# Kernel optimization log

Hardware: AMD Instinct MI355X
Metric: run time of the kernel (lower is better)

The kernel has to match this reference:

```python
import jax, jax.numpy as jnp
import numpy as np

ENCODER_DIM, DECODER_DIM, ATTENTION_DIM = 2048, 512, 512
B, L = 128, 196


def setup_inputs() -> dict:
    key = jax.random.key(0)
    ks = jax.random.split(key, 8)
    s_u = 1.0 / np.sqrt(ENCODER_DIM)
    s_w = 1.0 / np.sqrt(DECODER_DIM)
    s_a = 1.0 / np.sqrt(ATTENTION_DIM)
    return {
        "features": jax.random.normal(ks[0], (B, L, ENCODER_DIM), jnp.float32),
        "hidden_state": jax.random.normal(ks[1], (B, DECODER_DIM), jnp.float32),
        "U_w": jax.random.uniform(ks[2], (ENCODER_DIM, ATTENTION_DIM), jnp.float32, -s_u, s_u),
        "U_b": jax.random.uniform(ks[3], (ATTENTION_DIM,), jnp.float32, -s_u, s_u),
        "W_w": jax.random.uniform(ks[4], (DECODER_DIM, ATTENTION_DIM), jnp.float32, -s_w, s_w),
        "W_b": jax.random.uniform(ks[5], (ATTENTION_DIM,), jnp.float32, -s_w, s_w),
        "A_w": jax.random.uniform(ks[6], (ATTENTION_DIM,), jnp.float32, -s_a, s_a),
        "A_b": jax.random.uniform(ks[7], (1,), jnp.float32, -s_a, s_a),
    }


def reference(features, hidden_state, U_w, U_b, W_w, W_b, A_w, A_b):
    # u_hs: [B, L, A], w_ah: [B, A]
    u_hs = jnp.einsum('ble,ea->bla', features, U_w) + U_b
    w_ah = hidden_state @ W_w + W_b
    combined = jnp.tanh(u_hs + w_ah[:, None, :])          # [B, L, A]
    scores = jnp.einsum('bla,a->bl', combined, A_w) + A_b[0]  # [B, L]
    alpha = jax.nn.softmax(scores, axis=1)                 # [B, L]
    context = jnp.einsum('bl,ble->be', alpha, features)    # [B, E]
    return alpha, context
```

## Files before the change

### kernel.cpp

```cpp
#include <hip/hip_runtime.h>
#include <hip/hip_bf16.h>

#define ENC 2048
#define ADIM 512
#define DEC 512
#define NBATCH 128
#define NL 196
#define MTOT (NBATCH * NL)
#define NKT 64

typedef __attribute__((ext_vector_type(8))) short short8;
typedef __attribute__((ext_vector_type(4))) float f32x4;
typedef __attribute__((ext_vector_type(4))) unsigned int u32x4;

__device__ __forceinline__ unsigned short f2bf(float f) {
    __hip_bfloat16 h = __float2bfloat16(f);
    union { __hip_bfloat16 h; unsigned short u; } cv; cv.h = h; return cv.u;
}
__device__ __forceinline__ unsigned int f2bf2(float lo, float hi) {
    __hip_bfloat162 h = __float22bfloat162_rn(float2{lo, hi});
    union { __hip_bfloat162 h; unsigned int u; } cv; cv.h = h; return cv.u;
}

__device__ __forceinline__ void load_lds16(const void* g, void* l) {
    __builtin_amdgcn_global_load_lds(
        (const __attribute__((address_space(1))) unsigned int*)g,
        (__attribute__((address_space(3))) unsigned int*)l, 16, 0, 0);
}

__global__ void wah_kernel(const float* __restrict__ hidden, const float* __restrict__ Ww,
                           const float* __restrict__ Wb, float* __restrict__ wah) {
    __shared__ __align__(16) float hs[DEC];
    const int b = blockIdx.x, a = threadIdx.x;
    hs[a] = hidden[b * DEC + a];
    __syncthreads();
    float acc = Wb[a];
    #pragma unroll 4
    for (int d = 0; d < DEC; d += 4) {
        f32x4 h = *(const f32x4*)&hs[d];
        acc += h.x * Ww[(d    ) * ADIM + a];
        acc += h.y * Ww[(d + 1) * ADIM + a];
        acc += h.z * Ww[(d + 2) * ADIM + a];
        acc += h.w * Ww[(d + 3) * ADIM + a];
    }
    wah[b * ADIM + a] = acc;
}

__global__ void transpose_uw(const float* __restrict__ Uw, unsigned short* __restrict__ uwT) {
    __shared__ float t[32][33];
    const int k0 = blockIdx.x * 32, n0 = blockIdx.y * 32;
    const int tx = threadIdx.x, ty = threadIdx.y;
    #pragma unroll
    for (int i = 0; i < 4; ++i)
        t[ty + 8 * i][tx] = Uw[(size_t)(k0 + ty + 8 * i) * ADIM + n0 + tx];
    __syncthreads();
    #pragma unroll
    for (int i = 0; i < 4; ++i)
        uwT[(size_t)(n0 + ty + 8 * i) * ENC + k0 + tx] = f2bf(t[tx][ty + 8 * i]);
}

__global__ __launch_bounds__(256, 3) void gemm_score_kernel(
    const float* __restrict__ feat, const unsigned short* __restrict__ uwT,
    const float* __restrict__ Ub, const float* __restrict__ wahb,
    const float* __restrict__ Aw, float* __restrict__ part)
{
    __shared__ __align__(16) unsigned char Ab0[8192];
    __shared__ __align__(16) unsigned char Ab1[8192];
    __shared__ __align__(16) unsigned char Bb0[8192];
    __shared__ __align__(16) unsigned char Bb1[8192];

    const int tid  = threadIdx.x;
    const int lane = tid & 63;
    const int w    = tid >> 6;
    const int wr   = w >> 1, wc = w & 1;
    const int l15  = lane & 15, ldr = lane >> 4;

    const int bid  = blockIdx.x;
    const int work = (bid & 7) * 98 + (bid >> 3);
    const int mb   = work >> 2;
    const int nbk  = work & 3;

    const int r_ = tid >> 1, h_ = tid & 1;
    const float* aSrc = feat + (size_t)(mb * 128 + r_) * ENC + h_ * 16;
    const int xw = (r_ >> 1) & 3;
    const int wA0 = r_ * 64 + (((h_ * 2 + 0) ^ xw) << 4);
    const int wA1 = r_ * 64 + (((h_ * 2 + 1) ^ xw) << 4);

    const unsigned short* bSrc = uwT
        + (size_t)(nbk * 128 + w * 32 + (lane >> 2)) * ENC
        + ((lane & 3) ^ ((lane >> 3) & 3)) * 8;

    const int xr = (l15 >> 1) & 3;
    int abyte[4], bbyte[4];
    #pragma unroll
    for (int f = 0; f < 4; ++f) {
        const int r = wr * 64 + f * 16 + l15;
        const int n = wc * 64 + f * 16 + l15;
        abyte[f] = r * 64 + ((ldr ^ xr) << 4);
        bbyte[f] = n * 64 + ((ldr ^ xr) << 4);
    }

    f32x4 acc[4][4];
    #pragma unroll
    for (int i = 0; i < 4; ++i)
        #pragma unroll
        for (int j = 0; j < 4; ++j)
            acc[i][j] = (f32x4){0.f, 0.f, 0.f, 0.f};

    f32x4 a00, a01, a02, a03;
    f32x4 a10, a11, a12, a13;

#define ISSUE_A(KTI, R0, R1, R2, R3) {                                  \
    const f32x4* p = (const f32x4*)(aSrc + (size_t)(KTI) * 32);         \
    R0 = p[0]; R1 = p[1]; R2 = p[2]; R3 = p[3];                         \
    __builtin_amdgcn_sched_barrier(0);                                  \
}
#define ISSUE_B(KTI, BB) {                                              \
    load_lds16(bSrc + (size_t)(KTI) * 32,            (BB) + w * 2048);  \
    load_lds16(bSrc + 16 * ENC + (size_t)(KTI) * 32, (BB) + w * 2048 + 1024); \
    __builtin_amdgcn_sched_barrier(0);                                  \
}
#define CVT_WRITE(R0, R1, R2, R3, AB) {                                 \
    u32x4 w0, w1;                                                       \
    w0.x = f2bf2(R0.x, R0.y); w0.y = f2bf2(R0.z, R0.w);                 \
    w0.z = f2bf2(R1.x, R1.y); w0.w = f2bf2(R1.z, R1.w);                 \
    w1.x = f2bf2(R2.x, R2.y); w1.y = f2bf2(R2.z, R2.w);                 \
    w1.z = f2bf2(R3.x, R3.y); w1.w = f2bf2(R3.z, R3.w);                 \
    *(u32x4*)((AB) + wA0) = w0;                                         \
    *(u32x4*)((AB) + wA1) = w1;                                         \
}
#define COMPUTE(AB, BB) {                                               \
    short8 af[4], bf[4];                                                \
    _Pragma("unroll")                                                   \
    for (int f = 0; f < 4; ++f) {                                       \
        af[f] = *(const short8*)((AB) + abyte[f]);                      \
        bf[f] = *(const short8*)((BB) + bbyte[f]);                      \
    }                                                                   \
    _Pragma("unroll")                                                   \
    for (int fm = 0; fm < 4; ++fm)                                      \
        _Pragma("unroll")                                               \
        for (int fn = 0; fn < 4; ++fn)                                  \
            acc[fm][fn] = __builtin_amdgcn_mfma_f32_16x16x32_bf16(      \
                af[fm], bf[fn], acc[fm][fn], 0, 0, 0);                  \
}
#define PHASE(T2, RA0, RA1, RA2, RA3, AB, BB) {                         \
    CVT_WRITE(RA0, RA1, RA2, RA3, AB);                                  \
    ISSUE_A(T2, RA0, RA1, RA2, RA3);                                    \
    asm volatile("s_waitcnt vmcnt(10)");                                \
    __builtin_amdgcn_sched_barrier(0);                                  \
    asm volatile("s_waitcnt lgkmcnt(0)");                               \
    __builtin_amdgcn_sched_barrier(0);                                  \
    __builtin_amdgcn_s_barrier();                                       \
    COMPUTE(AB, BB);                                                    \
    __builtin_amdgcn_s_barrier();                                       \
    ISSUE_B(T2, BB);                                                    \
}

    ISSUE_A(0, a00, a01, a02, a03);
    ISSUE_B(0, Bb0);
    ISSUE_A(1, a10, a11, a12, a13);
    ISSUE_B(1, Bb1);

    #pragma unroll 1
    for (int kt = 0; kt < NKT; kt += 2) {
        const int k2 = (kt + 2 < NKT) ? kt + 2 : NKT - 1;
        const int k3 = (kt + 3 < NKT) ? kt + 3 : NKT - 1;
        PHASE(k2, a00, a01, a02, a03, Ab0, Bb0);
        PHASE(k3, a10, a11, a12, a13, Ab1, Bb1);
    }
#undef ISSUE_A
#undef ISSUE_B
#undef CVT_WRITE
#undef COMPUTE
#undef PHASE

    float ub4[4], aw4[4]; int cidx[4];
    #pragma unroll
    for (int f = 0; f < 4; ++f) {
        const int c = nbk * 128 + wc * 64 + f * 16 + l15;
        cidx[f] = c; ub4[f] = Ub[c]; aw4[f] = Aw[c];
    }
    #pragma unroll
    for (int fm = 0; fm < 4; ++fm) {
        #pragma unroll
        for (int r = 0; r < 4; ++r) {
            const int m = mb * 128 + wr * 64 + fm * 16 + ldr * 4 + r;
            const int b = m / NL;
            const float* wrow = wahb + b * ADIM;
            float s = 0.f;
            #pragma unroll
            for (int f = 0; f < 4; ++f)
                s += aw4[f] * tanhf(acc[fm][f][r] + ub4[f] + wrow[cidx[f]]);
            s += __shfl_xor(s, 1);
            s += __shfl_xor(s, 2);
            s += __shfl_xor(s, 4);
            s += __shfl_xor(s, 8);
            if (l15 == 0) part[(nbk * 2 + wc) * MTOT + m] = s;
        }
    }
}

__global__ void softmax_kernel(const float* __restrict__ part, const float* __restrict__ Ab,
                               float* __restrict__ alpha) {
    const int b = blockIdx.x, t = threadIdx.x;
    float sv = 0.f;
    if (t < NL) {
        sv = Ab[0];
        #pragma unroll
        for (int p = 0; p < 8; ++p) sv += part[p * MTOT + b * NL + t];
    }
    float v = (t < NL) ? sv : -3.4e38f;
    #pragma unroll
    for (int o = 32; o >= 1; o >>= 1) v = fmaxf(v, __shfl_xor(v, o));
    __shared__ float rm[4], rs[4];
    if ((t & 63) == 0) rm[t >> 6] = v;
    __syncthreads();
    const float bm = fmaxf(fmaxf(rm[0], rm[1]), fmaxf(rm[2], rm[3]));
    const float e = (t < NL) ? expf(sv - bm) : 0.f;
    float s = e;
    #pragma unroll
    for (int o = 32; o >= 1; o >>= 1) s += __shfl_xor(s, o);
    if ((t & 63) == 0) rs[t >> 6] = s;
    __syncthreads();
    const float bs = rs[0] + rs[1] + rs[2] + rs[3];
    if (t < NL) alpha[b * NL + t] = e / bs;
}

__global__ void context_kernel(const float* __restrict__ feat, const float* __restrict__ alpha,
                               float* __restrict__ ctx) {
    __shared__ float al[NL];
    const int b = blockIdx.x, chunk = blockIdx.y, t = threadIdx.x;
    for (int i = t; i < NL; i += 128) al[i] = alpha[b * NL + i];
    __syncthreads();
    const int e0 = chunk * 512 + t * 4;
    const float* fp = feat + (size_t)b * NL * ENC + e0;
    f32x4 acc0 = (f32x4){0.f, 0.f, 0.f, 0.f};
    f32x4 acc1 = (f32x4){0.f, 0.f, 0.f, 0.f};
    #pragma unroll 2
    for (int l = 0; l < NL; l += 2) {
        f32x4 f0 = *(const f32x4*)(fp + (size_t)l * ENC);
        f32x4 f1 = *(const f32x4*)(fp + (size_t)(l + 1) * ENC);
        acc0 += al[l] * f0;
        acc1 += al[l + 1] * f1;
    }
    f32x4 rsum = acc0 + acc1;
    *(f32x4*)(ctx + (size_t)b * ENC + e0) = rsum;
}

extern "C" void kernel_launch(void* const* d_in, const int* in_sizes, int n_in,
                              void* d_out, int out_size, void* d_ws, size_t ws_size,
                              hipStream_t stream) {
    const float* feat   = (const float*)d_in[0];
    const float* hidden = (const float*)d_in[1];
    const float* Uw     = (const float*)d_in[2];
    const float* Ub     = (const float*)d_in[3];
    const float* Ww     = (const float*)d_in[4];
    const float* Wb     = (const float*)d_in[5];
    const float* Aw     = (const float*)d_in[6];
    const float* Ab     = (const float*)d_in[7];

    float* out   = (float*)d_out;
    float* alpha = out;
    float* ctx   = out + MTOT;

    char* ws = (char*)d_ws;
    float*          wahb = (float*)ws;
    unsigned short* uwT  = (unsigned short*)(ws + 262144);
    float*          partb= (float*)(ws + 262144 + 2097152);

    wah_kernel<<<dim3(128), dim3(512), 0, stream>>>(hidden, Ww, Wb, wahb);
    transpose_uw<<<dim3(64, 16), dim3(32, 8), 0, stream>>>(Uw, uwT);
    gemm_score_kernel<<<dim3(784), dim3(256), 0, stream>>>(feat, uwT, Ub, wahb, Aw, partb);
    softmax_kernel<<<dim3(128), dim3(256), 0, stream>>>(partb, Ab, alpha);
    context_kernel<<<dim3(128, 4), dim3(128), 0, stream>>>(feat, alpha, ctx);
}
```

Before: 176.8 us.

## Double K-tile depth to 64 per stage with wider swizzle and MFMA priority

Widens the K tile of the fused GEMM+score kernel from 32 to 64 bf16 elements per stage. This halves the number of barrier/waitcnt iterations and doubles the loads in flight per phase. The LDS swizzle moves to an 8-chunk XOR pattern to match the 128-byte rows, and MFMA sections are bracketed with s_setprio. In exchange, LDS use doubles to 64KB and register pressure grows, so launch bounds drop from 3 to 2 blocks per CU, lowering occupancy.

```diff
diff --git a/kernel.cpp b/kernel.cpp
--- a/kernel.cpp
+++ b/kernel.cpp
@@ -7,7 +7,7 @@
 #define NBATCH 128
 #define NL 196
 #define MTOT (NBATCH * NL)
-#define NKT 64
+#define NKT 32
 
 typedef __attribute__((ext_vector_type(8))) short short8;
 typedef __attribute__((ext_vector_type(4))) float f32x4;
@@ -59,15 +59,15 @@
         uwT[(size_t)(n0 + ty + 8 * i) * ENC + k0 + tx] = f2bf(t[tx][ty + 8 * i]);
 }
 
-__global__ __launch_bounds__(256, 3) void gemm_score_kernel(
+__global__ __launch_bounds__(256, 2) void gemm_score_kernel(
     const float* __restrict__ feat, const unsigned short* __restrict__ uwT,
     const float* __restrict__ Ub, const float* __restrict__ wahb,
     const float* __restrict__ Aw, float* __restrict__ part)
 {
-    __shared__ __align__(16) unsigned char Ab0[8192];
-    __shared__ __align__(16) unsigned char Ab1[8192];
-    __shared__ __align__(16) unsigned char Bb0[8192];
-    __shared__ __align__(16) unsigned char Bb1[8192];
+    __shared__ __align__(16) unsigned char Ab0[16384];
+    __shared__ __align__(16) unsigned char Ab1[16384];
+    __shared__ __align__(16) unsigned char Bb0[16384];
+    __shared__ __align__(16) unsigned char Bb1[16384];
 
     const int tid  = threadIdx.x;
     const int lane = tid & 63;
@@ -81,23 +81,26 @@
     const int nbk  = work & 3;
 
     const int r_ = tid >> 1, h_ = tid & 1;
-    const float* aSrc = feat + (size_t)(mb * 128 + r_) * ENC + h_ * 16;
-    const int xw = (r_ >> 1) & 3;
-    const int wA0 = r_ * 64 + (((h_ * 2 + 0) ^ xw) << 4);
-    const int wA1 = r_ * 64 + (((h_ * 2 + 1) ^ xw) << 4);
+    const float* aSrc = feat + (size_t)(mb * 128 + r_) * ENC + h_ * 32;
+    int wA[4];
+    #pragma unroll
+    for (int j = 0; j < 4; ++j)
+        wA[j] = r_ * 128 + (((h_ * 4 + j) ^ (r_ & 7)) << 4);
 
     const unsigned short* bSrc = uwT
-        + (size_t)(nbk * 128 + w * 32 + (lane >> 2)) * ENC
-        + ((lane & 3) ^ ((lane >> 3) & 3)) * 8;
-
-    const int xr = (l15 >> 1) & 3;
-    int abyte[4], bbyte[4];
+        + (size_t)(nbk * 128 + w * 32 + (lane >> 3)) * ENC
+        + (((lane & 7) ^ ((lane >> 3) & 7)) << 3);
+
+    int abyte[4][2], bbyte[4][2];
     #pragma unroll
     for (int f = 0; f < 4; ++f) {
         const int r = wr * 64 + f * 16 + l15;
         const int n = wc * 64 + f * 16 + l15;
-        abyte[f] = r * 64 + ((ldr ^ xr) << 4);
-        bbyte[f] = n * 64 + ((ldr ^ xr) << 4);
+        #pragma unroll
+        for (int ks = 0; ks < 2; ++ks) {
+            abyte[f][ks] = r * 128 + (((ks * 4 + ldr) ^ (r & 7)) << 4);
+            bbyte[f][ks] = n * 128 + (((ks * 4 + ldr) ^ (n & 7)) << 4);
+        }
     }
 
     f32x4 acc[4][4];
@@ -107,46 +110,60 @@
         for (int j = 0; j < 4; ++j)
             acc[i][j] = (f32x4){0.f, 0.f, 0.f, 0.f};
 
-    f32x4 a00, a01, a02, a03;
-    f32x4 a10, a11, a12, a13;
-
-#define ISSUE_A(KTI, R0, R1, R2, R3) {                                  \
-    const f32x4* p = (const f32x4*)(aSrc + (size_t)(KTI) * 32);         \
+    f32x4 a00, a01, a02, a03, a04, a05, a06, a07;
+    f32x4 a10, a11, a12, a13, a14, a15, a16, a17;
+
+#define ISSUE_A(KTI, R0, R1, R2, R3, R4, R5, R6, R7) {                  \
+    const f32x4* p = (const f32x4*)(aSrc + (size_t)(KTI) * 64);         \
     R0 = p[0]; R1 = p[1]; R2 = p[2]; R3 = p[3];                         \
+    R4 = p[4]; R5 = p[5]; R6 = p[6]; R7 = p[7];                         \
     __builtin_amdgcn_sched_barrier(0);                                  \
 }
 #define ISSUE_B(KTI, BB) {                                              \
-    load_lds16(bSrc + (size_t)(KTI) * 32,            (BB) + w * 2048);  \
-    load_lds16(bSrc + 16 * ENC + (size_t)(KTI) * 32, (BB) + w * 2048 + 1024); \
-    __builtin_amdgcn_sched_barrier(0);                                  \
-}
-#define CVT_WRITE(R0, R1, R2, R3, AB) {                                 \
-    u32x4 w0, w1;                                                       \
+    _Pragma("unroll")                                                   \
+    for (int c = 0; c < 4; ++c)                                         \
+        load_lds16(bSrc + (size_t)(KTI) * 64 + c * 8 * ENC,             \
+                   (BB) + w * 4096 + c * 1024);                         \
+    __builtin_amdgcn_sched_barrier(0);                                  \
+}
+#define CVT_WRITE(R0, R1, R2, R3, R4, R5, R6, R7, AB) {                 \
+    u32x4 w0, w1, w2, w3;                                               \
     w0.x = f2bf2(R0.x, R0.y); w0.y = f2bf2(R0.z, R0.w);                 \
     w0.z = f2bf2(R1.x, R1.y); w0.w = f2bf2(R1.z, R1.w);                 \
     w1.x = f2bf2(R2.x, R2.y); w1.y = f2bf2(R2.z, R2.w);                 \
     w1.z = f2bf2(R3.x, R3.y); w1.w = f2bf2(R3.z, R3.w);                 \
-    *(u32x4*)((AB) + wA0) = w0;                                         \
-    *(u32x4*)((AB) + wA1) = w1;                                         \
+    w2.x = f2bf2(R4.x, R4.y); w2.y = f2bf2(R4.z, R4.w);                 \
+    w2.z = f2bf2(R5.x, R5.y); w2.w = f2bf2(R5.z, R5.w);                 \
+    w3.x = f2bf2(R6.x, R6.y); w3.y = f2bf2(R6.z, R6.w);                 \
+    w3.z = f2bf2(R7.x, R7.y); w3.w = f2bf2(R7.z, R7.w);                 \
+    *(u32x4*)((AB) + wA[0]) = w0;                                       \
+    *(u32x4*)((AB) + wA[1]) = w1;                                       \
+    *(u32x4*)((AB) + wA[2]) = w2;                                       \
+    *(u32x4*)((AB) + wA[3]) = w3;                                       \
 }
 #define COMPUTE(AB, BB) {                                               \
-    short8 af[4], bf[4];                                                \
+    __builtin_amdgcn_s_setprio(1);                                      \
     _Pragma("unroll")                                                   \
-    for (int f = 0; f < 4; ++f) {                                       \
-        af[f] = *(const short8*)((AB) + abyte[f]);                      \
-        bf[f] = *(const short8*)((BB) + bbyte[f]);                      \
+    for (int ks = 0; ks < 2; ++ks) {                                    \
+        short8 af[4], bf[4];                                            \
+        _Pragma("unroll")                                               \
+        for (int f = 0; f < 4; ++f) {                                   \
+            af[f] = *(const short8*)((AB) + abyte[f][ks]);              \
+            bf[f] = *(const short8*)((BB) + bbyte[f][ks]);              \
+        }                                                               \
+        _Pragma("unroll")                                               \
+        for (int fm = 0; fm < 4; ++fm)                                  \
+            _Pragma("unroll")                                           \
+            for (int fn = 0; fn < 4; ++fn)                              \
+                acc[fm][fn] = __builtin_amdgcn_mfma_f32_16x16x32_bf16(  \
+                    af[fm], bf[fn], acc[fm][fn], 0, 0, 0);              \
     }                                                                   \
-    _Pragma("unroll")                                                   \
-    for (int fm = 0; fm < 4; ++fm)                                      \
-        _Pragma("unroll")                                               \
-        for (int fn = 0; fn < 4; ++fn)                                  \
-            acc[fm][fn] = __builtin_amdgcn_mfma_f32_16x16x32_bf16(      \
-                af[fm], bf[fn], acc[fm][fn], 0, 0, 0);                  \
-}
-#define PHASE(T2, RA0, RA1, RA2, RA3, AB, BB) {                         \
-    CVT_WRITE(RA0, RA1, RA2, RA3, AB);                                  \
-    ISSUE_A(T2, RA0, RA1, RA2, RA3);                                    \
-    asm volatile("s_waitcnt vmcnt(10)");                                \
+    __builtin_amdgcn_s_setprio(0);                                      \
+}
+#define PHASE(T2, RA0, RA1, RA2, RA3, RA4, RA5, RA6, RA7, AB, BB) {     \
+    CVT_WRITE(RA0, RA1, RA2, RA3, RA4, RA5, RA6, RA7, AB);              \
+    ISSUE_A(T2, RA0, RA1, RA2, RA3, RA4, RA5, RA6, RA7);                \
+    asm volatile("s_waitcnt vmcnt(20)");                                \
     __builtin_amdgcn_sched_barrier(0);                                  \
     asm volatile("s_waitcnt lgkmcnt(0)");                               \
     __builtin_amdgcn_sched_barrier(0);                                  \
@@ -156,17 +173,17 @@
     ISSUE_B(T2, BB);                                                    \
 }
 
-    ISSUE_A(0, a00, a01, a02, a03);
+    ISSUE_A(0, a00, a01, a02, a03, a04, a05, a06, a07);
     ISSUE_B(0, Bb0);
-    ISSUE_A(1, a10, a11, a12, a13);
+    ISSUE_A(1, a10, a11, a12, a13, a14, a15, a16, a17);
     ISSUE_B(1, Bb1);
 
     #pragma unroll 1
     for (int kt = 0; kt < NKT; kt += 2) {
         const int k2 = (kt + 2 < NKT) ? kt + 2 : NKT - 1;
         const int k3 = (kt + 3 < NKT) ? kt + 3 : NKT - 1;
-        PHASE(k2, a00, a01, a02, a03, Ab0, Bb0);
-        PHASE(k3, a10, a11, a12, a13, Ab1, Bb1);
+        PHASE(k2, a00, a01, a02, a03, a04, a05, a06, a07, Ab0, Bb0);
+        PHASE(k3, a10, a11, a12, a13, a14, a15, a16, a17, Ab1, Bb1);
     }
 #undef ISSUE_A
 #undef ISSUE_B
```

Measured after the change: 232.0 us. +31.2%, slower.
